# Optimization experiments

Hardware: AMD Instinct MI355X
Metric: run time of the kernel (lower is better)

## Reference

```python
import jax, jax.numpy as jnp
import numpy as np

N_STRIDE = 128  # 'n' from __init__: stride between subsequences


def make_mask(S, m, n):
    # Faithful vectorization of create_mask: overlap of windows [i*n, i*n+m).
    # overlap_ratio = max(0, m - |i-j|*n) / m; mask True iff (0.5 <= ratio < 1) or i == j.
    # (ratio >= 1 only happens at i == j, which the first branch already catches.)
    idx = jnp.arange(S)
    diff = jnp.abs(idx[:, None] - idx[None, :])
    ratio = jnp.maximum(0, m - diff * n).astype(jnp.float32) / m
    return ((ratio >= 0.5) & (ratio < 1.0)) | (diff == 0)


def setup_inputs() -> dict:
    key = jax.random.key(0)
    k1, k2, k3 = jax.random.split(key, 3)
    B, D, S, L = 8, 8, 512, 256  # batch, num_dims, num_subsequences, seq_length(=d_model)
    x = jax.random.normal(k1, (B, D, S, L), jnp.float32)
    qkv_w = jax.random.normal(k2, (3 * L, L), jnp.float32) * (1.0 / np.sqrt(L))
    qkv_b = jax.random.normal(k3, (3 * L,), jnp.float32) * 0.02
    return {"x": x, "qkv_w": qkv_w, "qkv_b": qkv_b}


def reference(x, qkv_w, qkv_b):
    B, D, S, L = x.shape
    # Batched over the per-channel Python loop in the original.
    qkv = jnp.einsum('bdsl,ol->bdso', x, qkv_w) + qkv_b  # [B,D,S,3L]
    q, k, v = jnp.split(qkv, 3, axis=-1)
    attn = jnp.einsum('bdsh,bdth->bdst', q, k) / jnp.sqrt(jnp.float32(L))
    attn = jax.nn.softmax(attn, axis=-1)
    mask = make_mask(S, L, N_STRIDE)  # m = d_model = L
    attn = jnp.where(mask, jnp.float32(0), attn)  # masked_fill(mask, 0)
    out = jnp.einsum('bdst,bdth->bdsh', attn, v).reshape(B, D * S, L)
    # Block-diagonal scatter of per-channel attention maps: [B, D*S, D*S]
    z = jnp.zeros((B, D, S, D, S), attn.dtype)
    z = z.at[:, jnp.arange(D), :, jnp.arange(D), :].set(jnp.transpose(attn, (1, 0, 2, 3)))
    block = z.reshape(B, D * S, D * S)
    return out, block
```

## Files before the change

kernel.cpp:

```cpp
#include <hip/hip_runtime.h>

typedef unsigned short u16;
typedef __attribute__((ext_vector_type(8))) short bf16x8;
typedef __attribute__((ext_vector_type(4))) float f32x4;

#define NS 512
#define NL 256
#define NBD 64
#define OUT_ELEMS 8388608u

__device__ __forceinline__ u16 f2bf(float f) {
  union { float f; unsigned u; } v; v.f = f;
  unsigned u = v.u;
  unsigned r = (u + 0x7FFFu + ((u >> 16) & 1u)) >> 16;
  return (u16)r;
}

__device__ __forceinline__ bf16x8 pack8(float4 a, float4 b) {
  bf16x8 r;
  r[0] = (short)f2bf(a.x); r[1] = (short)f2bf(a.y);
  r[2] = (short)f2bf(a.z); r[3] = (short)f2bf(a.w);
  r[4] = (short)f2bf(b.x); r[5] = (short)f2bf(b.y);
  r[6] = (short)f2bf(b.z); r[7] = (short)f2bf(b.w);
  return r;
}

__device__ __forceinline__ bf16x8 pack8v(f32x4 a, f32x4 b) {
  bf16x8 r;
  r[0] = (short)f2bf(a[0]); r[1] = (short)f2bf(a[1]);
  r[2] = (short)f2bf(a[2]); r[3] = (short)f2bf(a[3]);
  r[4] = (short)f2bf(b[0]); r[5] = (short)f2bf(b[1]);
  r[6] = (short)f2bf(b[2]); r[7] = (short)f2bf(b[3]);
  return r;
}

__global__ __launch_bounds__(256) void qkv_kernel(
    const float* __restrict__ x, const float* __restrict__ w,
    const float* __restrict__ bias,
    u16* __restrict__ qws, u16* __restrict__ kws, u16* __restrict__ vws)
{
  __shared__ u16 wlds[64][264];

  const int t = threadIdx.x;
  const int wave = t >> 6, lane = t & 63;
  const int r16 = lane & 15, kg = lane >> 4;
  const int row0 = blockIdx.x * 64;
  const int srow = row0 + wave * 16 + r16;

  bf16x8 a[8];
  {
    const float* xr = x + (size_t)srow * NL;
    for (int ks = 0; ks < 8; ++ks) {
      float4 f0 = *(const float4*)(xr + ks * 32 + kg * 8);
      float4 f1 = *(const float4*)(xr + ks * 32 + kg * 8 + 4);
      a[ks] = pack8(f0, f1);
    }
  }

  const int wr = t >> 2, qq = t & 3;
  for (int ct = 0; ct < 12; ++ct) {
    const int col0 = ct * 64;
    __syncthreads();
    {
      const float* src = w + (size_t)(col0 + wr) * NL + qq * 64;
      u16* dst = &wlds[wr][qq * 64];
      for (int j = 0; j < 64; j += 8) {
        float4 f0 = *(const float4*)(src + j);
        float4 f1 = *(const float4*)(src + j + 4);
        *(bf16x8*)(void*)(dst + j) = pack8(f0, f1);
      }
    }
    __syncthreads();

    for (int cf = 0; cf < 4; ++cf) {
      const int cl = cf * 16 + r16;
      f32x4 acc = {0.f, 0.f, 0.f, 0.f};
      for (int ks = 0; ks < 8; ++ks) {
        bf16x8 b = *(const bf16x8*)(void*)&wlds[cl][ks * 32 + kg * 8];
        acc = __builtin_amdgcn_mfma_f32_16x16x32_bf16(a[ks], b, acc, 0, 0, 0);
      }
      const int o = col0 + cl;
      const float bv = bias[o];
      for (int i = 0; i < 4; ++i) {
        const float val = acc[i] + bv;
        const int grow = row0 + wave * 16 + kg * 4 + i;
        const int bd = grow >> 9, s = grow & 511;
        const u16 h = f2bf(val);
        if (o < 256)      qws[((size_t)bd * NS + s) * NL + o] = h;
        else if (o < 512) kws[((size_t)bd * NS + s) * NL + (o - 256)] = h;
        else              vws[((size_t)bd * NL + (o - 512)) * NS + s] = h;
      }
    }
  }
}

__global__ __launch_bounds__(256, 4) void attn_kernel(
    const u16* __restrict__ qws, const u16* __restrict__ kws,
    const u16* __restrict__ vws, float* __restrict__ out)
{
  __shared__ float Sm[16][516];
  __shared__ float rowinv[16];

  const int rt = blockIdx.x, bd = blockIdx.y;
  const int b = bd >> 3, d = bd & 7;
  const int t = threadIdx.x, wave = t >> 6, lane = t & 63;
  const int r16 = lane & 15, kg = lane >> 4;
  const size_t ch = (size_t)bd * NS * NL;
  const int row0 = rt * 16;

  bf16x8 aq[8];
  {
    const u16* p = qws + ch + (size_t)(row0 + r16) * NL + kg * 8;
    for (int ks = 0; ks < 8; ++ks)
      aq[ks] = *(const bf16x8*)(p + ks * 32);
  }

  for (int cf = 0; cf < 8; ++cf) {
    const int s2 = wave * 128 + cf * 16 + r16;
    const u16* p = kws + ch + (size_t)s2 * NL + kg * 8;
    f32x4 acc = {0, 0, 0, 0};
    for (int ks = 0; ks < 8; ++ks) {
      bf16x8 bfr = *(const bf16x8*)(p + ks * 32);
      acc = __builtin_amdgcn_mfma_f32_16x16x32_bf16(aq[ks], bfr, acc, 0, 0, 0);
    }
    const int c = wave * 128 + cf * 16 + r16;
    for (int i = 0; i < 4; ++i)
      Sm[kg * 4 + i][c] = acc[i] * 0.0625f;
  }
  __syncthreads();

  {
    const int row = wave * 4 + (lane >> 4);
    const int c16 = lane & 15;
    float m = -1e30f;
    for (int j = 0; j < 32; ++j)
      m = fmaxf(m, Sm[row][c16 + j * 16]);
    m = fmaxf(m, __shfl_xor(m, 1));
    m = fmaxf(m, __shfl_xor(m, 2));
    m = fmaxf(m, __shfl_xor(m, 4));
    m = fmaxf(m, __shfl_xor(m, 8));
    float s = 0.f;
    for (int j = 0; j < 32; ++j) {
      const int c = c16 + j * 16;
      const float e = __expf(Sm[row][c] - m);
      Sm[row][c] = e;
      s += e;
    }
    s += __shfl_xor(s, 1);
    s += __shfl_xor(s, 2);
    s += __shfl_xor(s, 4);
    s += __shfl_xor(s, 8);
    if (c16 == 0) rowinv[row] = 1.0f / s;
  }
  __syncthreads();

  for (int k = 0; k < 8; ++k) {
    const int slot = t + k * 256;
    const int row = slot >> 7, c4 = slot & 127;
    const float inv = rowinv[row];
    const int s1g = row0 + row;
    f32x4 e4 = *(const f32x4*)&Sm[row][c4 * 4];
    f32x4 p;
    for (int u = 0; u < 4; ++u) {
      const int c = c4 * 4 + u;
      const int dd = c > s1g ? c - s1g : s1g - c;
      p[u] = (dd <= 1) ? 0.f : e4[u] * inv;
    }
    *(f32x4*)&Sm[row][c4 * 4] = p;
    float* brow = out + OUT_ELEMS + ((size_t)b << 24) +
                  (size_t)(d * NS + s1g) * 4096 + d * NS;
    __builtin_nontemporal_store(p, (f32x4*)brow + c4);
  }
  __syncthreads();

  f32x4 accO[4];
  for (int cf = 0; cf < 4; ++cf) accO[cf] = (f32x4){0, 0, 0, 0};
  for (int ks = 0; ks < 16; ++ks) {
    const float* p = &Sm[r16][ks * 32 + kg * 8];
    bf16x8 pa = pack8v(*(const f32x4*)p, *(const f32x4*)(p + 4));
    for (int cf = 0; cf < 4; ++cf) {
      const int f = wave * 64 + cf * 16 + r16;
      bf16x8 bv = *(const bf16x8*)(vws + ((size_t)bd * NL + f) * NS + ks * 32 + kg * 8);
      accO[cf] = __builtin_amdgcn_mfma_f32_16x16x32_bf16(pa, bv, accO[cf], 0, 0, 0);
    }
  }
  for (int cf = 0; cf < 4; ++cf) {
    const int fcol = wave * 64 + cf * 16 + r16;
    for (int i = 0; i < 4; ++i) {
      const int s1 = row0 + kg * 4 + i;
      __builtin_nontemporal_store(accO[cf][i],
          out + (size_t)b * (4096u * 256u) + (size_t)(d * NS + s1) * NL + fcol);
    }
  }

  {
    const f32x4 z4 = {0.f, 0.f, 0.f, 0.f};
    float* base = out + OUT_ELEMS + ((size_t)b << 24) +
                  (size_t)(d * NS + row0) * 4096;
    const int dlo = d << 7;
    for (int idx = t; idx < 16 * 1024; idx += 256) {
      const int row = idx >> 10, c4 = idx & 1023;
      if ((unsigned)(c4 - dlo) >= 128u)
        __builtin_nontemporal_store(z4, (f32x4*)(base + (size_t)row * 4096) + c4);
    }
  }
}

extern "C" void kernel_launch(void* const* d_in, const int* in_sizes, int n_in,
                              void* d_out, int out_size, void* d_ws, size_t ws_size,
                              hipStream_t stream) {
  const float* x    = (const float*)d_in[0];
  const float* w    = (const float*)d_in[1];
  const float* bias = (const float*)d_in[2];
  float* out = (float*)d_out;

  u16* qws = (u16*)d_ws;
  u16* kws = qws + (size_t)NBD * NS * NL;
  u16* vws = kws + (size_t)NBD * NS * NL;

  qkv_kernel<<<dim3(512), 256, 0, stream>>>(x, w, bias, qws, kws, vws);
  attn_kernel<<<dim3(32, 64), 256, 0, stream>>>(qws, kws, vws, out);
}
```

Measured before the change: 297.4 us.

## Enlarge attention row tile to 64 rows with 512-thread blocks and early zero-fill

Each attention block now handles 64 query rows with 8 waves instead of 16 rows with 4 waves. K and V fragments loaded from global memory are reused across four 16-row sub-tiles, which cuts K/V reload traffic fourfold. The zero-fill of the off-diagonal block output moves to the start of the kernel so those stores can overlap with the compute. The cost is higher register pressure (four Q fragment sets and eight accumulators), about 132 KB of LDS per block, and fewer blocks in flight.

```diff
diff --git a/kernel.cpp b/kernel.cpp
--- a/kernel.cpp
+++ b/kernel.cpp
@@ -94,54 +94,66 @@
   }
 }
 
-__global__ __launch_bounds__(256, 4) void attn_kernel(
+__global__ __launch_bounds__(512, 2) void attn_kernel(
     const u16* __restrict__ qws, const u16* __restrict__ kws,
     const u16* __restrict__ vws, float* __restrict__ out)
 {
-  __shared__ float Sm[16][516];
-  __shared__ float rowinv[16];
+  __shared__ float Sm[64][516];
+  __shared__ float rowinv[64];
 
   const int rt = blockIdx.x, bd = blockIdx.y;
   const int b = bd >> 3, d = bd & 7;
   const int t = threadIdx.x, wave = t >> 6, lane = t & 63;
   const int r16 = lane & 15, kg = lane >> 4;
   const size_t ch = (size_t)bd * NS * NL;
-  const int row0 = rt * 16;
-
-  bf16x8 aq[8];
+  const int row0 = rt * 64;
+
   {
-    const u16* p = qws + ch + (size_t)(row0 + r16) * NL + kg * 8;
+    const f32x4 z4 = {0.f, 0.f, 0.f, 0.f};
+    float* base = out + OUT_ELEMS + ((size_t)b << 24) +
+                  (size_t)(d * NS + row0) * 4096;
+    const int dlo = d << 7;
+    for (int idx = t; idx < 64 * 1024; idx += 512) {
+      const int row = idx >> 10, c4 = idx & 1023;
+      if ((unsigned)(c4 - dlo) >= 128u)
+        __builtin_nontemporal_store(z4, (f32x4*)(base + (size_t)row * 4096) + c4);
+    }
+  }
+
+  bf16x8 aq[4][8];
+  for (int rf = 0; rf < 4; ++rf) {
+    const u16* p = qws + ch + (size_t)(row0 + rf * 16 + r16) * NL + kg * 8;
     for (int ks = 0; ks < 8; ++ks)
-      aq[ks] = *(const bf16x8*)(p + ks * 32);
-  }
-
-  for (int cf = 0; cf < 8; ++cf) {
-    const int s2 = wave * 128 + cf * 16 + r16;
+      aq[rf][ks] = *(const bf16x8*)(p + ks * 32);
+  }
+
+  for (int cf = 0; cf < 4; ++cf) {
+    const int s2 = wave * 64 + cf * 16 + r16;
     const u16* p = kws + ch + (size_t)s2 * NL + kg * 8;
-    f32x4 acc = {0, 0, 0, 0};
-    for (int ks = 0; ks < 8; ++ks) {
-      bf16x8 bfr = *(const bf16x8*)(p + ks * 32);
-      acc = __builtin_amdgcn_mfma_f32_16x16x32_bf16(aq[ks], bfr, acc, 0, 0, 0);
-    }
-    const int c = wave * 128 + cf * 16 + r16;
-    for (int i = 0; i < 4; ++i)
-      Sm[kg * 4 + i][c] = acc[i] * 0.0625f;
+    bf16x8 bfr[8];
+    for (int ks = 0; ks < 8; ++ks)
+      bfr[ks] = *(const bf16x8*)(p + ks * 32);
+    for (int rf = 0; rf < 4; ++rf) {
+      f32x4 acc = {0.f, 0.f, 0.f, 0.f};
+      for (int ks = 0; ks < 8; ++ks)
+        acc = __builtin_amdgcn_mfma_f32_16x16x32_bf16(aq[rf][ks], bfr[ks], acc, 0, 0, 0);
+      for (int i = 0; i < 4; ++i)
+        Sm[rf * 16 + kg * 4 + i][s2] = acc[i] * 0.0625f;
+    }
   }
   __syncthreads();
 
   {
-    const int row = wave * 4 + (lane >> 4);
-    const int c16 = lane & 15;
+    const int row = t >> 3, c8 = t & 7;
     float m = -1e30f;
-    for (int j = 0; j < 32; ++j)
-      m = fmaxf(m, Sm[row][c16 + j * 16]);
+    for (int j = 0; j < 64; ++j)
+      m = fmaxf(m, Sm[row][c8 + j * 8]);
     m = fmaxf(m, __shfl_xor(m, 1));
     m = fmaxf(m, __shfl_xor(m, 2));
     m = fmaxf(m, __shfl_xor(m, 4));
-    m = fmaxf(m, __shfl_xor(m, 8));
     float s = 0.f;
-    for (int j = 0; j < 32; ++j) {
-      const int c = c16 + j * 16;
+    for (int j = 0; j < 64; ++j) {
+      const int c = c8 + j * 8;
       const float e = __expf(Sm[row][c] - m);
       Sm[row][c] = e;
       s += e;
@@ -149,13 +161,12 @@
     s += __shfl_xor(s, 1);
     s += __shfl_xor(s, 2);
     s += __shfl_xor(s, 4);
-    s += __shfl_xor(s, 8);
-    if (c16 == 0) rowinv[row] = 1.0f / s;
+    if (c8 == 0) rowinv[row] = 1.0f / s;
   }
   __syncthreads();
 
-  for (int k = 0; k < 8; ++k) {
-    const int slot = t + k * 256;
+  for (int k = 0; k < 16; ++k) {
+    const int slot = t + k * 512;
     const int row = slot >> 7, c4 = slot & 127;
     const float inv = rowinv[row];
     const int s1g = row0 + row;
@@ -173,37 +184,31 @@
   }
   __syncthreads();
 
-  f32x4 accO[4];
-  for (int cf = 0; cf < 4; ++cf) accO[cf] = (f32x4){0, 0, 0, 0};
+  f32x4 accO[4][2];
+  for (int rf = 0; rf < 4; ++rf)
+    for (int cf = 0; cf < 2; ++cf) accO[rf][cf] = (f32x4){0, 0, 0, 0};
   for (int ks = 0; ks < 16; ++ks) {
-    const float* p = &Sm[r16][ks * 32 + kg * 8];
-    bf16x8 pa = pack8v(*(const f32x4*)p, *(const f32x4*)(p + 4));
-    for (int cf = 0; cf < 4; ++cf) {
-      const int f = wave * 64 + cf * 16 + r16;
+    bf16x8 pa[4];
+    for (int rf = 0; rf < 4; ++rf) {
+      const float* p = &Sm[rf * 16 + r16][ks * 32 + kg * 8];
+      pa[rf] = pack8v(*(const f32x4*)p, *(const f32x4*)(p + 4));
+    }
+    for (int cf = 0; cf < 2; ++cf) {
+      const int f = wave * 32 + cf * 16 + r16;
       bf16x8 bv = *(const bf16x8*)(vws + ((size_t)bd * NL + f) * NS + ks * 32 + kg * 8);
-      accO[cf] = __builtin_amdgcn_mfma_f32_16x16x32_bf16(pa, bv, accO[cf], 0, 0, 0);
-    }
-  }
-  for (int cf = 0; cf < 4; ++cf) {
-    const int fcol = wave * 64 + cf * 16 + r16;
-    for (int i = 0; i < 4; ++i) {
-      const int s1 = row0 + kg * 4 + i;
-      __builtin_nontemporal_store(accO[cf][i],
-          out + (size_t)b * (4096u * 256u) + (size_t)(d * NS + s1) * NL + fcol);
-    }
-  }
-
-  {
-    const f32x4 z4 = {0.f, 0.f, 0.f, 0.f};
-    float* base = out + OUT_ELEMS + ((size_t)b << 24) +
-                  (size_t)(d * NS + row0) * 4096;
-    const int dlo = d << 7;
-    for (int idx = t; idx < 16 * 1024; idx += 256) {
-      const int row = idx >> 10, c4 = idx & 1023;
-      if ((unsigned)(c4 - dlo) >= 128u)
-        __builtin_nontemporal_store(z4, (f32x4*)(base + (size_t)row * 4096) + c4);
-    }
-  }
+      for (int rf = 0; rf < 4; ++rf)
+        accO[rf][cf] = __builtin_amdgcn_mfma_f32_16x16x32_bf16(pa[rf], bv, accO[rf][cf], 0, 0, 0);
+    }
+  }
+  for (int rf = 0; rf < 4; ++rf)
+    for (int cf = 0; cf < 2; ++cf) {
+      const int fcol = wave * 32 + cf * 16 + r16;
+      for (int i = 0; i < 4; ++i) {
+        const int s1 = row0 + rf * 16 + kg * 4 + i;
+        __builtin_nontemporal_store(accO[rf][cf][i],
+            out + (size_t)b * (4096u * 256u) + (size_t)(d * NS + s1) * NL + fcol);
+      }
+    }
 }
 
 extern "C" void kernel_launch(void* const* d_in, const int* in_sizes, int n_in,
@@ -219,5 +224,5 @@
   u16* vws = kws + (size_t)NBD * NS * NL;
 
   qkv_kernel<<<dim3(512), 256, 0, stream>>>(x, w, bias, qws, kws, vws);
-  attn_kernel<<<dim3(32, 64), 256, 0, stream>>>(qws, kws, vws, out);
-}
+  attn_kernel<<<dim3(8, 64), 512, 0, stream>>>(qws, kws, vws, out);
+}
```

Result: faster. 270.1 us (-9.2%).
